# Performance work log

Hardware: AMD Instinct MI355X
Metric: run time of the kernel (lower is better)

Reference implementation:

```python
import jax, jax.numpy as jnp
import numpy as np

B, S, E = 2, 2048, 2048
H, DH = 16, 128          # n_head, head_dim
ROT = 32                 # rotary_dim (partial RoPE)
MP = 8                   # mp_num in original forward
MASKED_BIAS = -1e9


def setup_inputs() -> dict:
    key = jax.random.key(0)
    k1, k2, k3 = jax.random.split(key, 3)
    hidden_states = jax.random.normal(k1, (B, S, E), dtype=jnp.float32)
    W_qkv = jax.random.normal(k2, (3 * E, E), dtype=jnp.float32) * (E ** -0.5)
    W_out = jax.random.normal(k3, (E, E), dtype=jnp.float32) * (E ** -0.5)
    return {"hidden_states": hidden_states, "W_qkv": W_qkv, "W_out": W_out}


def _rope_sincos(seq_len, rot_dim, dtype):
    inv_freq = 1.0 / (10000.0 ** (jnp.arange(0, rot_dim, 2, dtype=jnp.float32) / rot_dim))
    ang = jnp.arange(seq_len, dtype=jnp.float32)[:, None] * inv_freq[None, :]  # [S, R/2]
    return jnp.sin(ang).astype(dtype), jnp.cos(ang).astype(dtype)


def _apply_rope(x, sin, cos):
    # x: [B,S,H,R]; sin/cos: [S,R/2] -> repeat_interleave(2) -> [S,R]
    sin2 = jnp.repeat(sin, 2, axis=-1)[None, :, None, :]
    cos2 = jnp.repeat(cos, 2, axis=-1)[None, :, None, :]
    x1 = x[..., ::2]
    x2 = x[..., 1::2]
    rot = jnp.stack((-x2, x1), axis=-1).reshape(x.shape)  # rotate_every_two
    return x * cos2 + rot * sin2


def reference(hidden_states, W_qkv, W_out):
    b, s, e = hidden_states.shape
    # qkv_proj (no bias): torch Linear does x @ W^T
    qkv = jnp.einsum('bse,fe->bsf', hidden_states, W_qkv)          # [B,S,3E]
    qkv = qkv.reshape(b, s, MP, 3 * e // MP)
    q, k, v = jnp.split(qkv, 3, axis=-1)                            # each [B,S,MP,E/MP]
    # _split_heads: flatten mp dim, re-split into heads
    q = q.reshape(b, s, H, DH)
    k = k.reshape(b, s, H, DH)
    v = v.reshape(b, s, H, DH)
    # partial rotary on first ROT dims (q,k in [B,S,H,DH] layout)
    sin, cos = _rope_sincos(s, ROT, hidden_states.dtype)
    q = jnp.concatenate([_apply_rope(q[..., :ROT], sin, cos), q[..., ROT:]], axis=-1)
    k = jnp.concatenate([_apply_rope(k[..., :ROT], sin, cos), k[..., ROT:]], axis=-1)
    # attention: scores / sqrt(DH), causal masked_fill(-1e9), softmax, AV
    scale = jnp.sqrt(jnp.asarray(DH, dtype=jnp.float32)).astype(hidden_states.dtype)
    scores = jnp.einsum('bqhd,bkhd->bhqk', q, k) / scale            # [B,H,S,S]
    causal = jnp.tril(jnp.ones((s, s), dtype=bool))
    scores = jnp.where(causal[None, None], scores, jnp.asarray(MASKED_BIAS, scores.dtype))
    attn = jax.nn.softmax(scores, axis=-1)
    out = jnp.einsum('bhqk,bkhd->bqhd', attn, v)                    # [B,S,H,DH]
    out = out.reshape(b, s, e)
    return jnp.einsum('bse,fe->bsf', out, W_out)                    # out_proj
```

## Files before the change

### kernel.cpp

```cpp
#include <hip/hip_runtime.h>
#include <hip/hip_bf16.h>
#include <cstdint>
#include <cstddef>

using bf16 = __hip_bfloat16;
using short4v = __attribute__((ext_vector_type(4))) short;
using short8 = __attribute__((ext_vector_type(8))) short;
using floatx4 = __attribute__((ext_vector_type(4))) float;

#define MFMA_BF16(A, B, C) __builtin_amdgcn_mfma_f32_16x16x32_bf16((A), (B), (C), 0, 0, 0)

__device__ inline short bf16_bits(float x) {
  bf16 v = __float2bfloat16(x);
  short r;
  __builtin_memcpy(&r, &v, 2);
  return r;
}

__device__ inline void store_c(bf16* p, float v) { *p = __float2bfloat16(v); }
__device__ inline void store_c(float* p, float v) { *p = v; }

__global__ __launch_bounds__(256) void f32_to_bf16_kernel(
    const float* __restrict__ src, bf16* __restrict__ dst, int n8) {
  const int i = blockIdx.x * 256 + threadIdx.x;
  if (i >= n8) return;
  const float4 a = ((const float4*)src)[2 * i];
  const float4 b = ((const float4*)src)[2 * i + 1];
  short8 r;
  r[0] = bf16_bits(a.x); r[1] = bf16_bits(a.y); r[2] = bf16_bits(a.z); r[3] = bf16_bits(a.w);
  r[4] = bf16_bits(b.x); r[5] = bf16_bits(b.y); r[6] = bf16_bits(b.z); r[7] = bf16_bits(b.w);
  *(short8*)(dst + (size_t)i * 8) = r;
}

template <typename TC>
__global__ __launch_bounds__(256) void gemm_bt_async(
    const bf16* __restrict__ A, const bf16* __restrict__ B, TC* __restrict__ C,
    int ldc, int K, bf16* __restrict__ vT, int mpbase) {
  __shared__ bf16 As[128 * 64];
  __shared__ bf16 Bs[128 * 64];
  const int tid = threadIdx.x;
  const int lane = tid & 63;
  const int wave = tid >> 6;
  const int lrow = lane & 15;
  const int quad = lane >> 4;
  const int wm = (wave >> 1) * 64;
  const int wn = (wave & 1) * 64;
  const int tm = blockIdx.y * 128;
  const int tn = blockIdx.x * 128;

  const int srow = tid >> 3;
  const int scl = tid & 7;

  floatx4 acc[4][4] = {};

  for (int k0 = 0; k0 < K; k0 += 64) {
    __syncthreads();
#pragma unroll
    for (int r = 0; r < 4; ++r) {
      const int row = r * 32 + srow;
      const int scg = scl ^ (row & 7);
      __builtin_amdgcn_global_load_lds(
          (const __attribute__((address_space(1))) void*)(A + (size_t)(tm + row) * K + k0 + scg * 8),
          (__attribute__((address_space(3))) void*)(As + row * 64 + scl * 8), 16, 0, 0);
    }
#pragma unroll
    for (int r = 0; r < 4; ++r) {
      const int row = r * 32 + srow;
      const int scg = scl ^ (row & 7);
      __builtin_amdgcn_global_load_lds(
          (const __attribute__((address_space(1))) void*)(B + (size_t)(tn + row) * K + k0 + scg * 8),
          (__attribute__((address_space(3))) void*)(Bs + row * 64 + scl * 8), 16, 0, 0);
    }
    __syncthreads();

#pragma unroll
    for (int kk = 0; kk < 2; ++kk) {
      short8 af[4], bfr[4];
#pragma unroll
      for (int i = 0; i < 4; ++i) {
        const int ra = wm + i * 16 + lrow;
        const int rb = wn + i * 16 + lrow;
        af[i] = *(const short8*)&As[ra * 64 + (((kk * 4 + quad) ^ (ra & 7)) * 8)];
        bfr[i] = *(const short8*)&Bs[rb * 64 + (((kk * 4 + quad) ^ (rb & 7)) * 8)];
      }
#pragma unroll
      for (int i = 0; i < 4; ++i)
#pragma unroll
        for (int j = 0; j < 4; ++j)
          acc[i][j] = MFMA_BF16(af[i], bfr[j], acc[i][j]);
    }
  }

  if (vT != nullptr && ((int)blockIdx.x % 6) >= 4) {
    const int mpl = (int)blockIdx.x / 6;
#pragma unroll
    for (int i = 0; i < 4; ++i)
#pragma unroll
      for (int j = 0; j < 4; ++j) {
        const int fl = tn + wn + j * 16 + lrow;
        const int sv = fl - mpl * 768 - 512;
        const int hh = mpbase + mpl * 2 + (sv >> 7);
        const int dd = sv & 127;
        const int m0 = tm + wm + i * 16 + quad * 4;
        const int bb = m0 >> 11;
        const int ss = m0 & 2047;
        short4v pv;
        pv[0] = bf16_bits(acc[i][j][0]); pv[1] = bf16_bits(acc[i][j][1]);
        pv[2] = bf16_bits(acc[i][j][2]); pv[3] = bf16_bits(acc[i][j][3]);
        *(short4v*)&vT[((size_t)(bb * 16 + hh) * 128 + dd) * 2048 + ss] = pv;
      }
  } else {
#pragma unroll
    for (int i = 0; i < 4; ++i)
#pragma unroll
      for (int j = 0; j < 4; ++j)
#pragma unroll
        for (int r = 0; r < 4; ++r) {
          const int row = tm + wm + i * 16 + quad * 4 + r;
          const int col = tn + wn + j * 16 + lrow;
          store_c(&C[(size_t)row * ldc + col], acc[i][j][r]);
        }
  }
}

__global__ __launch_bounds__(256) void gemm_abf16_bf32(
    const bf16* __restrict__ A, const float* __restrict__ B, float* __restrict__ C,
    int ldc, int K) {
  __shared__ bf16 As[128 * 64];
  __shared__ bf16 Bs[128 * 64];
  const int tid = threadIdx.x;
  const int lane = tid & 63;
  const int wave = tid >> 6;
  const int lrow = lane & 15;
  const int quad = lane >> 4;
  const int wm = (wave >> 1) * 64;
  const int wn = (wave & 1) * 64;
  const int tm = blockIdx.y * 128;
  const int tn = blockIdx.x * 128;

  const int srow = tid >> 3;
  const int scl = tid & 7;
  const int c16 = tid & 15;
  const int br0 = tid >> 4;

  floatx4 acc[4][4] = {};
  float4 breg[8];
#pragma unroll
  for (int r = 0; r < 8; ++r)
    breg[r] = *(const float4*)(B + (size_t)(tn + r * 16 + br0) * K + c16 * 4);

  for (int k0 = 0; k0 < K; k0 += 64) {
    __syncthreads();
#pragma unroll
    for (int r = 0; r < 4; ++r) {
      const int row = r * 32 + srow;
      const int scg = scl ^ (row & 7);
      __builtin_amdgcn_global_load_lds(
          (const __attribute__((address_space(1))) void*)(A + (size_t)(tm + row) * K + k0 + scg * 8),
          (__attribute__((address_space(3))) void*)(As + row * 64 + scl * 8), 16, 0, 0);
    }
#pragma unroll
    for (int r = 0; r < 8; ++r) {
      const int row = r * 16 + br0;
      short4v sv;
      sv[0] = bf16_bits(breg[r].x); sv[1] = bf16_bits(breg[r].y);
      sv[2] = bf16_bits(breg[r].z); sv[3] = bf16_bits(breg[r].w);
      *(short4v*)&Bs[row * 64 + (((c16 >> 1) ^ (row & 7)) * 8) + (c16 & 1) * 4] = sv;
    }
    __syncthreads();
    if (k0 + 64 < K) {
#pragma unroll
      for (int r = 0; r < 8; ++r)
        breg[r] = *(const float4*)(B + (size_t)(tn + r * 16 + br0) * K + k0 + 64 + c16 * 4);
    }

#pragma unroll
    for (int kk = 0; kk < 2; ++kk) {
      short8 af[4], bfr[4];
#pragma unroll
      for (int i = 0; i < 4; ++i) {
        const int ra = wm + i * 16 + lrow;
        const int rb = wn + i * 16 + lrow;
        af[i] = *(const short8*)&As[ra * 64 + (((kk * 4 + quad) ^ (ra & 7)) * 8)];
        bfr[i] = *(const short8*)&Bs[rb * 64 + (((kk * 4 + quad) ^ (rb & 7)) * 8)];
      }
#pragma unroll
      for (int i = 0; i < 4; ++i)
#pragma unroll
        for (int j = 0; j < 4; ++j)
          acc[i][j] = MFMA_BF16(af[i], bfr[j], acc[i][j]);
    }
  }

#pragma unroll
  for (int i = 0; i < 4; ++i)
#pragma unroll
    for (int j = 0; j < 4; ++j)
#pragma unroll
      for (int r = 0; r < 4; ++r) {
        const int row = tm + wm + i * 16 + quad * 4 + r;
        const int col = tn + wn + j * 16 + lrow;
        C[(size_t)row * ldc + col] = acc[i][j][r];
      }
}

__global__ void rope_kernel(bf16* __restrict__ qkv) {
  const int idx = blockIdx.x * 256 + threadIdx.x;
  const int i = idx & 15;
  int t = idx >> 4;
  const int qk = t & 1;
  t >>= 1;
  const int h = t & 15;
  t >>= 4;
  const int s = t & 2047;
  bf16* p = qkv + (size_t)t * 6144 + (h >> 1) * 768 + (h & 1) * 128 + qk * 256 + 2 * i;
  const float x0 = __bfloat162float(p[0]);
  const float x1 = __bfloat162float(p[1]);
  const float inv = powf(10000.f, -(float)(2 * i) / 32.f);
  const float ang = (float)s * inv;
  float sn, cs;
  sincosf(ang, &sn, &cs);
  p[0] = __float2bfloat16(x0 * cs - x1 * sn);
  p[1] = __float2bfloat16(x1 * cs + x0 * sn);
}

__global__ __launch_bounds__(256) void attn_flash_pair(
    const bf16* __restrict__ qkv, const bf16* __restrict__ vT,
    bf16* __restrict__ out) {
  __shared__ short Ks[16 * 64 * 8];
  __shared__ short Vs[8 * 128 * 8];
  __shared__ short Ps[8 * 128 * 8];
  const int tid = threadIdx.x;
  const int wave = tid >> 6;
  const int lane = tid & 63;
  const int lq = lane & 15;
  const int quad = lane >> 4;
  const int h = blockIdx.y;
  const int b = blockIdx.z;
  const size_t SROW = 6144;
  const bf16* base = qkv + (size_t)b * 2048 * SROW;
  const int qoff = (h >> 1) * 768 + (h & 1) * 128;
  const int koff = qoff + 256;
  const float scale = 0.088388347648318447f;

  const int sr = tid >> 2;
  const int sq = tid & 3;
  const bf16* kbase = base + (size_t)sr * SROW + koff + sq * 32;

  const bf16* vrow = vT + (size_t)(b * 16 + h) * 262144 +
                     (size_t)(tid >> 1) * 2048 + (tid & 1) * 32;
  short* vdst = &Vs[(((tid & 1) * 4) * 128 + (tid >> 1)) * 8];

  short8 kv[4], vv[4];
#pragma unroll
  for (int j = 0; j < 4; ++j) kv[j] = *(const short8*)(kbase + j * 8);
#pragma unroll
  for (int i = 0; i < 4; ++i) vv[i] = *(const short8*)(vrow + i * 8);

  for (int phase = 0; phase < 2; ++phase) {
    const int qb = phase ? (15 - (int)blockIdx.x) : (int)blockIdx.x;

    short8 qf[2][4];
#pragma unroll
    for (int rt = 0; rt < 2; ++rt) {
      const bf16* qp =
          base + (size_t)(qb * 128 + wave * 32 + rt * 16 + lq) * SROW + qoff + quad * 8;
#pragma unroll
      for (int ks = 0; ks < 4; ++ks) qf[rt][ks] = *(const short8*)(qp + ks * 32);
    }

    floatx4 o[2][8] = {};
    float m_i[2] = {-1e30f, -1e30f};
    float l_i[2] = {0.f, 0.f};

    const int kb_end = 2 * qb + 2;
    for (int kb = 0; kb < kb_end; ++kb) {
      __syncthreads();

#pragma unroll
      for (int j = 0; j < 4; ++j) *(short8*)&Ks[((sq * 4 + j) * 64 + sr) * 8] = kv[j];
#pragma unroll
      for (int i = 0; i < 4; ++i) *(short8*)(vdst + i * 1024) = vv[i];
      __syncthreads();

      {
        const bool last = (kb + 1 == kb_end);
        const bool pf = !last || (phase == 0);
        const int nkb = !last ? kb + 1 : 0;
        if (pf) {
          const size_t koffg = (size_t)nkb * 64 * SROW;
          const int voffg = nkb * 64;
#pragma unroll
          for (int j = 0; j < 4; ++j) kv[j] = *(const short8*)(kbase + koffg + j * 8);
#pragma unroll
          for (int i = 0; i < 4; ++i) vv[i] = *(const short8*)(vrow + voffg + i * 8);
        }
      }

      floatx4 sc[2][4] = {};
      __builtin_amdgcn_s_setprio(1);
#pragma unroll
      for (int ks = 0; ks < 4; ++ks) {
        short8 kf[4];
#pragma unroll
        for (int ct = 0; ct < 4; ++ct)
          kf[ct] = *(const short8*)&Ks[((ks * 4 + quad) * 64 + ct * 16 + lq) * 8];
#pragma unroll
        for (int rt = 0; rt < 2; ++rt)
#pragma unroll
          for (int ct = 0; ct < 4; ++ct)
            sc[rt][ct] = MFMA_BF16(kf[ct], qf[rt][ks], sc[rt][ct]);
      }
      __builtin_amdgcn_s_setprio(0);

      const int qrow0 = qb * 128 + wave * 32;
      const bool diag = (kb * 64 + 63 > qrow0);
#pragma unroll
      for (int rt = 0; rt < 2; ++rt) {
        const int qg = qrow0 + rt * 16 + lq;
#pragma unroll
        for (int ct = 0; ct < 4; ++ct)
#pragma unroll
          for (int r = 0; r < 4; ++r) {
            float v = sc[rt][ct][r] * scale;
            if (diag && (kb * 64 + ct * 16 + quad * 4 + r) > qg) v = -1e9f;
            sc[rt][ct][r] = v;
          }
        float c0 = fmaxf(fmaxf(sc[rt][0][0], sc[rt][0][1]), fmaxf(sc[rt][0][2], sc[rt][0][3]));
        float c1 = fmaxf(fmaxf(sc[rt][1][0], sc[rt][1][1]), fmaxf(sc[rt][1][2], sc[rt][1][3]));
        float c2 = fmaxf(fmaxf(sc[rt][2][0], sc[rt][2][1]), fmaxf(sc[rt][2][2], sc[rt][2][3]));
        float c3 = fmaxf(fmaxf(sc[rt][3][0], sc[rt][3][1]), fmaxf(sc[rt][3][2], sc[rt][3][3]));
        float mx = fmaxf(fmaxf(c0, c1), fmaxf(c2, c3));
        mx = fmaxf(mx, __shfl_xor(mx, 16, 64));
        mx = fmaxf(mx, __shfl_xor(mx, 32, 64));
        float mnew = m_i[rt];
        if (!__all(mx <= mnew)) {
          mnew = fmaxf(mnew, mx);
          const float alpha = __expf(m_i[rt] - mnew);
          m_i[rt] = mnew;
          l_i[rt] *= alpha;
#pragma unroll
          for (int dt = 0; dt < 8; ++dt) o[rt][dt] *= alpha;
        }
        float s0 = 0.f, s1 = 0.f, s2 = 0.f, s3 = 0.f;
#pragma unroll
        for (int ct = 0; ct < 4; ++ct) {
          const float p0 = __expf(sc[rt][ct][0] - mnew);
          const float p1 = __expf(sc[rt][ct][1] - mnew);
          const float p2 = __expf(sc[rt][ct][2] - mnew);
          const float p3 = __expf(sc[rt][ct][3] - mnew);
          sc[rt][ct][0] = p0; sc[rt][ct][1] = p1; sc[rt][ct][2] = p2; sc[rt][ct][3] = p3;
          s0 += p0; s1 += p1; s2 += p2; s3 += p3;
        }
        float rs = (s0 + s1) + (s2 + s3);
        rs += __shfl_xor(rs, 16, 64);
        rs += __shfl_xor(rs, 32, 64);
        l_i[rt] += rs;
        const int prow = wave * 32 + rt * 16 + lq;
#pragma unroll
        for (int ct = 0; ct < 4; ++ct) {
          short4v pv;
          pv[0] = bf16_bits(sc[rt][ct][0]); pv[1] = bf16_bits(sc[rt][ct][1]);
          pv[2] = bf16_bits(sc[rt][ct][2]); pv[3] = bf16_bits(sc[rt][ct][3]);
          const int kgrp = ct * 2 + (quad >> 1);
          *(short4v*)&Ps[(kgrp * 128 + prow) * 8 + (quad & 1) * 4] = pv;
        }
      }

      __builtin_amdgcn_s_setprio(1);
#pragma unroll
      for (int kk = 0; kk < 2; ++kk) {
        short8 pf[2], vf[8];
#pragma unroll
        for (int rt = 0; rt < 2; ++rt)
          pf[rt] = *(const short8*)&Ps[((kk * 4 + quad) * 128 + wave * 32 + rt * 16 + lq) * 8];
#pragma unroll
        for (int dt = 0; dt < 8; ++dt)
          vf[dt] = *(const short8*)&Vs[((kk * 4 + quad) * 128 + dt * 16 + lq) * 8];
#pragma unroll
        for (int rt = 0; rt < 2; ++rt)
#pragma unroll
          for (int dt = 0; dt < 8; ++dt)
            o[rt][dt] = MFMA_BF16(vf[dt], pf[rt], o[rt][dt]);
      }
      __builtin_amdgcn_s_setprio(0);
    }

#pragma unroll
    for (int rt = 0; rt < 2; ++rt) {
      const float inv_l = 1.f / l_i[rt];
      const int qg = qb * 128 + wave * 32 + rt * 16 + lq;
      bf16* op = out + ((size_t)(b * 2048 + qg)) * 2048 + h * 128 + quad * 4;
#pragma unroll
      for (int dt = 0; dt < 8; ++dt) {
        short4v s4;
        s4[0] = bf16_bits(o[rt][dt][0] * inv_l);
        s4[1] = bf16_bits(o[rt][dt][1] * inv_l);
        s4[2] = bf16_bits(o[rt][dt][2] * inv_l);
        s4[3] = bf16_bits(o[rt][dt][3] * inv_l);
        *(short4v*)(op + dt * 16) = s4;
      }
    }
  }
}

extern "C" void kernel_launch(void* const* d_in, const int* in_sizes, int n_in,
                              void* d_out, int out_size, void* d_ws, size_t ws_size,
                              hipStream_t stream) {
  const float* hidden = (const float*)d_in[0];
  const float* Wqkv = (const float*)d_in[1];
  const float* Wout = (const float*)d_in[2];
  float* outp = (float*)d_out;

  bf16* qkv = (bf16*)d_ws;
  bf16* flex = qkv + (size_t)4096 * 6144;
  bf16* hbf = (bf16*)d_out;
  bf16* vT = (bf16*)d_out + (size_t)8 * 1024 * 1024;

  f32_to_bf16_kernel<<<4096, 256, 0, stream>>>(hidden, hbf, 1048576);

  f32_to_bf16_kernel<<<3072, 256, 0, stream>>>(Wqkv, flex, 786432);
  gemm_bt_async<bf16><<<dim3(24, 32), 256, 0, stream>>>(hbf, flex, qkv, 6144, 2048, vT, 0);
  f32_to_bf16_kernel<<<3072, 256, 0, stream>>>(Wqkv + (size_t)3072 * 2048, flex, 786432);
  gemm_bt_async<bf16><<<dim3(24, 32), 256, 0, stream>>>(hbf, flex, qkv + 3072, 6144, 2048, vT, 8);

  rope_kernel<<<8192, 256, 0, stream>>>(qkv);

  bf16* attnout = flex;
  attn_flash_pair<<<dim3(8, 16, 2), 256, 0, stream>>>(qkv, vT, attnout);

  gemm_abf16_bf32<<<dim3(16, 32), 256, 0, stream>>>(attnout, Wout, outp, 2048, 2048);
}
```

Before: 435.4 us.

## Use 128-key tiles with direct global-to-LDS loads in flash attention

The flash attention kernel now processes 128-key blocks instead of 64, so there are half as many iterations and barriers per query block. K and V tiles are loaded directly into LDS with global_load_lds instead of the old register prefetch-and-store path. This removes the overlap that prefetching gave, so loads are now exposed between the two barriers. The softmax scale is folded into the exponent instead of being applied to every score, and the row-sum shuffle reduction moves out of the loop to the final normalization. LDS use roughly doubles, which may lower occupancy.

```diff
diff --git a/kernel.cpp b/kernel.cpp
--- a/kernel.cpp
+++ b/kernel.cpp
@@ -227,9 +227,9 @@
 __global__ __launch_bounds__(256) void attn_flash_pair(
     const bf16* __restrict__ qkv, const bf16* __restrict__ vT,
     bf16* __restrict__ out) {
-  __shared__ short Ks[16 * 64 * 8];
-  __shared__ short Vs[8 * 128 * 8];
-  __shared__ short Ps[8 * 128 * 8];
+  __shared__ short Ks[16 * 128 * 8];
+  __shared__ short Vs[16 * 128 * 8];
+  __shared__ short Ps[16 * 128 * 8];
   const int tid = threadIdx.x;
   const int wave = tid >> 6;
   const int lane = tid & 63;
@@ -239,24 +239,11 @@
   const int b = blockIdx.z;
   const size_t SROW = 6144;
   const bf16* base = qkv + (size_t)b * 2048 * SROW;
+  const bf16* vbase = vT + (size_t)(b * 16 + h) * 262144;
   const int qoff = (h >> 1) * 768 + (h & 1) * 128;
   const int koff = qoff + 256;
   const float scale = 0.088388347648318447f;
 
-  const int sr = tid >> 2;
-  const int sq = tid & 3;
-  const bf16* kbase = base + (size_t)sr * SROW + koff + sq * 32;
-
-  const bf16* vrow = vT + (size_t)(b * 16 + h) * 262144 +
-                     (size_t)(tid >> 1) * 2048 + (tid & 1) * 32;
-  short* vdst = &Vs[(((tid & 1) * 4) * 128 + (tid >> 1)) * 8];
-
-  short8 kv[4], vv[4];
-#pragma unroll
-  for (int j = 0; j < 4; ++j) kv[j] = *(const short8*)(kbase + j * 8);
-#pragma unroll
-  for (int i = 0; i < 4; ++i) vv[i] = *(const short8*)(vrow + i * 8);
-
   for (int phase = 0; phase < 2; ++phase) {
     const int qb = phase ? (15 - (int)blockIdx.x) : (int)blockIdx.x;
 
@@ -271,94 +258,92 @@
 
     floatx4 o[2][8] = {};
     float m_i[2] = {-1e30f, -1e30f};
-    float l_i[2] = {0.f, 0.f};
-
-    const int kb_end = 2 * qb + 2;
+    float l_acc[2] = {0.f, 0.f};
+
+    const int kb_end = qb + 1;
     for (int kb = 0; kb < kb_end; ++kb) {
       __syncthreads();
 
 #pragma unroll
-      for (int j = 0; j < 4; ++j) *(short8*)&Ks[((sq * 4 + j) * 64 + sr) * 8] = kv[j];
-#pragma unroll
-      for (int i = 0; i < 4; ++i) *(short8*)(vdst + i * 1024) = vv[i];
+      for (int i = 0; i < 8; ++i) {
+        const int u = wave * 8 + i;
+        const int g = u >> 1;
+        const int half = (u & 1) * 64;
+        __builtin_amdgcn_global_load_lds(
+            (const __attribute__((address_space(1))) void*)(
+                base + (size_t)(kb * 128 + half + lane) * SROW + koff + g * 8),
+            (__attribute__((address_space(3))) void*)(Ks + (g * 128 + half + lane) * 8),
+            16, 0, 0);
+        __builtin_amdgcn_global_load_lds(
+            (const __attribute__((address_space(1))) void*)(
+                vbase + (size_t)(half + lane) * 2048 + kb * 128 + g * 8),
+            (__attribute__((address_space(3))) void*)(Vs + (g * 128 + half + lane) * 8),
+            16, 0, 0);
+      }
       __syncthreads();
 
-      {
-        const bool last = (kb + 1 == kb_end);
-        const bool pf = !last || (phase == 0);
-        const int nkb = !last ? kb + 1 : 0;
-        if (pf) {
-          const size_t koffg = (size_t)nkb * 64 * SROW;
-          const int voffg = nkb * 64;
-#pragma unroll
-          for (int j = 0; j < 4; ++j) kv[j] = *(const short8*)(kbase + koffg + j * 8);
-#pragma unroll
-          for (int i = 0; i < 4; ++i) vv[i] = *(const short8*)(vrow + voffg + i * 8);
-        }
-      }
-
-      floatx4 sc[2][4] = {};
+      floatx4 sc[2][8] = {};
       __builtin_amdgcn_s_setprio(1);
 #pragma unroll
       for (int ks = 0; ks < 4; ++ks) {
-        short8 kf[4];
-#pragma unroll
-        for (int ct = 0; ct < 4; ++ct)
-          kf[ct] = *(const short8*)&Ks[((ks * 4 + quad) * 64 + ct * 16 + lq) * 8];
+        const int dg = ks * 4 + quad;
+        short8 kf[8];
+#pragma unroll
+        for (int ct = 0; ct < 8; ++ct)
+          kf[ct] = *(const short8*)&Ks[(dg * 128 + ct * 16 + lq) * 8];
 #pragma unroll
         for (int rt = 0; rt < 2; ++rt)
 #pragma unroll
-          for (int ct = 0; ct < 4; ++ct)
+          for (int ct = 0; ct < 8; ++ct)
             sc[rt][ct] = MFMA_BF16(kf[ct], qf[rt][ks], sc[rt][ct]);
       }
       __builtin_amdgcn_s_setprio(0);
 
       const int qrow0 = qb * 128 + wave * 32;
-      const bool diag = (kb * 64 + 63 > qrow0);
+      const bool diag = (kb == qb);
 #pragma unroll
       for (int rt = 0; rt < 2; ++rt) {
         const int qg = qrow0 + rt * 16 + lq;
-#pragma unroll
-        for (int ct = 0; ct < 4; ++ct)
-#pragma unroll
-          for (int r = 0; r < 4; ++r) {
-            float v = sc[rt][ct][r] * scale;
-            if (diag && (kb * 64 + ct * 16 + quad * 4 + r) > qg) v = -1e9f;
-            sc[rt][ct][r] = v;
-          }
-        float c0 = fmaxf(fmaxf(sc[rt][0][0], sc[rt][0][1]), fmaxf(sc[rt][0][2], sc[rt][0][3]));
-        float c1 = fmaxf(fmaxf(sc[rt][1][0], sc[rt][1][1]), fmaxf(sc[rt][1][2], sc[rt][1][3]));
-        float c2 = fmaxf(fmaxf(sc[rt][2][0], sc[rt][2][1]), fmaxf(sc[rt][2][2], sc[rt][2][3]));
-        float c3 = fmaxf(fmaxf(sc[rt][3][0], sc[rt][3][1]), fmaxf(sc[rt][3][2], sc[rt][3][3]));
-        float mx = fmaxf(fmaxf(c0, c1), fmaxf(c2, c3));
+        if (diag) {
+#pragma unroll
+          for (int ct = 0; ct < 8; ++ct)
+#pragma unroll
+            for (int r = 0; r < 4; ++r)
+              if (kb * 128 + ct * 16 + quad * 4 + r > qg) sc[rt][ct][r] = -1e9f;
+        }
+        float cm[8];
+#pragma unroll
+        for (int ct = 0; ct < 8; ++ct)
+          cm[ct] = fmaxf(fmaxf(sc[rt][ct][0], sc[rt][ct][1]),
+                         fmaxf(sc[rt][ct][2], sc[rt][ct][3]));
+        float mx = fmaxf(fmaxf(fmaxf(cm[0], cm[1]), fmaxf(cm[2], cm[3])),
+                         fmaxf(fmaxf(cm[4], cm[5]), fmaxf(cm[6], cm[7])));
         mx = fmaxf(mx, __shfl_xor(mx, 16, 64));
         mx = fmaxf(mx, __shfl_xor(mx, 32, 64));
-        float mnew = m_i[rt];
-        if (!__all(mx <= mnew)) {
-          mnew = fmaxf(mnew, mx);
-          const float alpha = __expf(m_i[rt] - mnew);
+        float mcur = m_i[rt];
+        if (!__all(mx <= mcur)) {
+          const float mnew = fmaxf(mcur, mx);
+          const float alpha = __expf((mcur - mnew) * scale);
           m_i[rt] = mnew;
-          l_i[rt] *= alpha;
+          mcur = mnew;
+          l_acc[rt] *= alpha;
 #pragma unroll
           for (int dt = 0; dt < 8; ++dt) o[rt][dt] *= alpha;
         }
         float s0 = 0.f, s1 = 0.f, s2 = 0.f, s3 = 0.f;
 #pragma unroll
-        for (int ct = 0; ct < 4; ++ct) {
-          const float p0 = __expf(sc[rt][ct][0] - mnew);
-          const float p1 = __expf(sc[rt][ct][1] - mnew);
-          const float p2 = __expf(sc[rt][ct][2] - mnew);
-          const float p3 = __expf(sc[rt][ct][3] - mnew);
+        for (int ct = 0; ct < 8; ++ct) {
+          const float p0 = __expf((sc[rt][ct][0] - mcur) * scale);
+          const float p1 = __expf((sc[rt][ct][1] - mcur) * scale);
+          const float p2 = __expf((sc[rt][ct][2] - mcur) * scale);
+          const float p3 = __expf((sc[rt][ct][3] - mcur) * scale);
           sc[rt][ct][0] = p0; sc[rt][ct][1] = p1; sc[rt][ct][2] = p2; sc[rt][ct][3] = p3;
           s0 += p0; s1 += p1; s2 += p2; s3 += p3;
         }
-        float rs = (s0 + s1) + (s2 + s3);
-        rs += __shfl_xor(rs, 16, 64);
-        rs += __shfl_xor(rs, 32, 64);
-        l_i[rt] += rs;
+        l_acc[rt] += (s0 + s1) + (s2 + s3);
         const int prow = wave * 32 + rt * 16 + lq;
 #pragma unroll
-        for (int ct = 0; ct < 4; ++ct) {
+        for (int ct = 0; ct < 8; ++ct) {
           short4v pv;
           pv[0] = bf16_bits(sc[rt][ct][0]); pv[1] = bf16_bits(sc[rt][ct][1]);
           pv[2] = bf16_bits(sc[rt][ct][2]); pv[3] = bf16_bits(sc[rt][ct][3]);
@@ -369,7 +354,7 @@
 
       __builtin_amdgcn_s_setprio(1);
 #pragma unroll
-      for (int kk = 0; kk < 2; ++kk) {
+      for (int kk = 0; kk < 4; ++kk) {
         short8 pf[2], vf[8];
 #pragma unroll
         for (int rt = 0; rt < 2; ++rt)
@@ -388,7 +373,10 @@
 
 #pragma unroll
     for (int rt = 0; rt < 2; ++rt) {
-      const float inv_l = 1.f / l_i[rt];
+      float l = l_acc[rt];
+      l += __shfl_xor(l, 16, 64);
+      l += __shfl_xor(l, 32, 64);
+      const float inv_l = 1.f / l;
       const int qg = qb * 128 + wave * 32 + rt * 16 + lq;
       bf16* op = out + ((size_t)(b * 2048 + qg)) * 2048 + h * 128 + quad * 4;
 #pragma unroll
```

Result: no change. 432.8 us (-0.6%).
